# Kernel optimization log

Hardware: AMD Instinct MI355X
Metric: run time of the kernel (lower is better)

## Reference

```python
import jax, jax.numpy as jnp
import numpy as np

N = 50000   # nodes
E = 600000  # edges
D = 128     # in = hidden = out channels (must be equal per the cat/mean readout)
B = 4096    # number of lookup indices


def setup_inputs() -> dict:
    key = jax.random.key(0)
    ks = jax.random.split(key, 8)
    x = jax.random.normal(ks[0], (N, D), dtype=jnp.float32)
    edge_index = jax.random.randint(ks[1], (2, E), 0, N)
    edge_weight = jax.random.uniform(ks[2], (E,), dtype=jnp.float32)
    inputs_idx = jax.random.randint(ks[3], (B,), 0, N + 1)  # N is the appended zero row
    def lin_w(k, din, dout):
        return jax.random.normal(k, (din, dout), dtype=jnp.float32) / np.sqrt(din).astype(np.float32)
    W1 = lin_w(ks[4], D, D); b1 = jnp.zeros((D,), jnp.float32)
    W2 = lin_w(ks[5], D, D); b2 = jnp.zeros((D,), jnp.float32)
    W3 = lin_w(ks[6], D, D); b3 = jnp.zeros((D,), jnp.float32)
    return {"inputs_idx": inputs_idx, "x": x, "edge_index": edge_index,
            "edge_weight": edge_weight, "W1": W1, "b1": b1, "W2": W2,
            "b2": b2, "W3": W3, "b3": b3}


def gcn_conv(x, W, b, src, dst, w):
    # PyG GCNConv with add_self_loops=True (fill weight 1) and symmetric norm.
    deg = jnp.zeros((N,), x.dtype).at[dst].add(w) + 1.0  # self-loop contributes 1
    dinv = jax.lax.rsqrt(deg)
    norm = dinv[src] * w * dinv[dst]                      # [E]
    h = x @ W                                             # [N, D]
    agg = jax.ops.segment_sum(norm[:, None] * h[src], dst, num_segments=N)
    agg = agg + h * (dinv * dinv)[:, None]                # self-loop term: deg^-1 * h
    return agg + b


def lookup(x, inputs_idx):
    # append a zero row, then gather
    x_ = jnp.concatenate([x, jnp.zeros((1, x.shape[-1]), x.dtype)], axis=0)
    return x_[inputs_idx]  # [B, D]


def reference(inputs_idx, x, edge_index, edge_weight, W1, b1, W2, b2, W3, b3):
    src, dst = edge_index[0], edge_index[1]
    x1 = jax.nn.relu(gcn_conv(x, W1, b1, src, dst, edge_weight))
    x2 = jax.nn.relu(gcn_conv(x1, W2, b2, src, dst, edge_weight))
    x3 = jax.nn.relu(gcn_conv(x2, W3, b3, src, dst, edge_weight))
    e1 = lookup(x1, inputs_idx)
    e2 = lookup(x2, inputs_idx)
    e3 = lookup(x3, inputs_idx)
    # torch.cat([1,B,D]x3, dim=0).mean(0) == elementwise mean of the three
    return (e1 + e2 + e3) / 3.0
```

## Files before the change

### kernel.cpp

```cpp
#include <hip/hip_runtime.h>
#include <hip/hip_fp16.h>

#define D 128
#define STRIDE 48

typedef _Float16 f16x8 __attribute__((ext_vector_type(8)));
typedef float f32x4 __attribute__((ext_vector_type(4)));
struct h4 { __half2 a, b; };

__global__ __launch_bounds__(256) void zero_kernel(int* __restrict__ p, int n) {
  int i = blockIdx.x * 256 + threadIdx.x;
  if (i < n) p[i] = 0;
}

__global__ __launch_bounds__(256) void build_kernel(
    const int* __restrict__ ei, const float* __restrict__ ew,
    int* __restrict__ cnt, int2* __restrict__ pairs, int E) {
  int e = blockIdx.x * 256 + threadIdx.x;
  if (e >= E) return;
  int s = ei[e], d = ei[E + e];
  int rank = atomicAdd(&cnt[d], 1);
  if (rank < STRIDE) pairs[(size_t)d * STRIDE + rank] = make_int2(s, __float_as_int(ew[e]));
}

__global__ __launch_bounds__(256) void deg_dinv_kernel(
    int* __restrict__ cnt, const int2* __restrict__ pairs,
    float* __restrict__ dinv, int N) {
  int n = blockIdx.x * 4 + (threadIdx.x >> 6);
  int lane = threadIdx.x & 63;
  if (n >= N) return;
  int c = cnt[n];
  c = c < STRIDE ? c : STRIDE;
  float v = (lane < c) ? __int_as_float(pairs[(size_t)n * STRIDE + lane].y) : 0.f;
#pragma unroll
  for (int o = 32; o > 0; o >>= 1) v += __shfl_xor(v, o, 64);
  if (lane == 0) {
    dinv[n] = rsqrtf(v + 1.0f);
    cnt[n] = c;
  }
}

__global__ __launch_bounds__(256) void norm_kernel(
    const int* __restrict__ cnt, const float* __restrict__ dinv,
    int2* __restrict__ pairs, int N) {
  int n = blockIdx.x * 4 + (threadIdx.x >> 6);
  int lane = threadIdx.x & 63;
  if (n >= N) return;
  int c = cnt[n];
  float di = dinv[n];
  if (lane < c) {
    int2 p = pairs[(size_t)n * STRIDE + lane];
    p.y = __float_as_int(dinv[p.x] * __int_as_float(p.y) * di);
    pairs[(size_t)n * STRIDE + lane] = p;
  }
}

__global__ __launch_bounds__(256) void tohalf_kernel(
    const float* __restrict__ in, __half* __restrict__ out, int n4) {
  int t = blockIdx.x * 256 + threadIdx.x;
  if (t >= n4) return;
  float4 v = ((const float4*)in)[t];
  h4 o = {__floats2half2_rn(v.x, v.y), __floats2half2_rn(v.z, v.w)};
  ((h4*)out)[t] = o;
}

__global__ __launch_bounds__(256) void wtrans_kernel(
    const float* __restrict__ W1, const float* __restrict__ W2,
    const float* __restrict__ W3, __half* __restrict__ WT1,
    __half* __restrict__ WT2, __half* __restrict__ WT3) {
  int t = blockIdx.x * 256 + threadIdx.x;
  if (t >= 3 * D * D) return;
  int m = t >> 14;
  int i = t & (D * D - 1);
  int k = i >> 7, n = i & 127;
  const float* W = (m == 0) ? W1 : (m == 1) ? W2 : W3;
  __half* WT = (m == 0) ? WT1 : (m == 1) ? WT2 : WT3;
  WT[n * D + k] = __float2half(W[k * D + n]);
}

__global__ __launch_bounds__(256) void agg_kernel(
    const __half* __restrict__ x16, const float* __restrict__ dinv,
    const int* __restrict__ cnt, const int2* __restrict__ pairs,
    __half* __restrict__ agg16, int N) {
  int gw = (blockIdx.x * 256 + threadIdx.x) >> 6;
  int lane = threadIdx.x & 63;
  if (gw >= N) return;
  const __half2* xs = (const __half2*)x16;
  float di = dinv[gw];
  int c = cnt[gw];
  const int2* pr = pairs + (size_t)gw * STRIDE;
  float2 acc = __half22float2(xs[(size_t)gw * 64 + lane]);
  acc.x *= di * di;
  acc.y *= di * di;
  int e = 0;
  for (; e + 4 <= c; e += 4) {
    int2 p0 = pr[e], p1 = pr[e + 1], p2 = pr[e + 2], p3 = pr[e + 3];
    float n0 = __int_as_float(p0.y), n1 = __int_as_float(p1.y);
    float n2 = __int_as_float(p2.y), n3 = __int_as_float(p3.y);
    float2 v0 = __half22float2(xs[(size_t)p0.x * 64 + lane]);
    float2 v1 = __half22float2(xs[(size_t)p1.x * 64 + lane]);
    float2 v2 = __half22float2(xs[(size_t)p2.x * 64 + lane]);
    float2 v3 = __half22float2(xs[(size_t)p3.x * 64 + lane]);
    acc.x += n0 * v0.x + n1 * v1.x + n2 * v2.x + n3 * v3.x;
    acc.y += n0 * v0.y + n1 * v1.y + n2 * v2.y + n3 * v3.y;
  }
  for (; e < c; e++) {
    int2 p0 = pr[e];
    float n0 = __int_as_float(p0.y);
    float2 v0 = __half22float2(xs[(size_t)p0.x * 64 + lane]);
    acc.x += n0 * v0.x;
    acc.y += n0 * v0.y;
  }
  ((__half2*)agg16)[(size_t)gw * 64 + lane] = __floats2half2_rn(acc.x, acc.y);
}

__global__ __launch_bounds__(256) void gemm16(
    const __half* __restrict__ A16, const __half* __restrict__ WT,
    const float* __restrict__ bias, __half* __restrict__ out16, int n) {
  __shared__ __half Bs[D * D];
  const int tid = threadIdx.x;
  const int wid = tid >> 6;
  const int lane = tid & 63;
  const int l15 = lane & 15;
  const int lk = lane >> 4;
  const int rbase = blockIdx.x * 64 + wid * 16;

  f16x8 a[4];
  {
    int r = rbase + l15;
    bool ok = (r < n);
    const __half* arow = A16 + (size_t)r * D + lk * 8;
#pragma unroll
    for (int kk = 0; kk < 4; kk++) {
      f16x8 z = {0, 0, 0, 0, 0, 0, 0, 0};
      a[kk] = ok ? *(const f16x8*)(arow + kk * 32) : z;
    }
  }
  {
    const int4* src = (const int4*)WT;
#pragma unroll
    for (int i = 0; i < 8; i++) {
      int slot = tid + i * 256;
      int byte = slot << 4;
      int row = byte >> 8;
      int4 v = src[slot];
      *(int4*)((char*)Bs + (byte ^ ((row & 7) << 4))) = v;
    }
  }
  __syncthreads();

  f32x4 c[8];
#pragma unroll
  for (int nf = 0; nf < 8; nf++) c[nf] = (f32x4){0.f, 0.f, 0.f, 0.f};

#pragma unroll
  for (int kk = 0; kk < 4; kk++) {
#pragma unroll
    for (int nf = 0; nf < 8; nf++) {
      int byte = ((nf * 16 + l15) << 8) + (kk << 6) + (lk << 4);
      byte ^= (l15 & 7) << 4;
      f16x8 b = *(const f16x8*)((const char*)Bs + byte);
      c[nf] = __builtin_amdgcn_mfma_f32_16x16x32_f16(a[kk], b, c[nf], 0, 0, 0);
    }
  }

#pragma unroll
  for (int nf = 0; nf < 8; nf++) {
    float bv = bias[nf * 16 + l15];
    int r0 = rbase + lk * 4;
#pragma unroll
    for (int rg = 0; rg < 4; rg++) {
      int r = r0 + rg;
      if (r < n) {
        float v = fmaxf(c[nf][rg] + bv, 0.f);
        out16[(size_t)r * D + nf * 16 + l15] = __float2half(v);
      }
    }
  }
}

__global__ __launch_bounds__(256) void lookup_kernel(
    const __half* __restrict__ xl, const int* __restrict__ idx,
    float* __restrict__ out, int B, int N, int add) {
  int t = blockIdx.x * 256 + threadIdx.x;
  if (t >= B * 16) return;
  int b = t >> 4, c8 = t & 15;
  int id = idx[b];
  float4 o0 = make_float4(0.f, 0.f, 0.f, 0.f);
  float4 o1 = make_float4(0.f, 0.f, 0.f, 0.f);
  if ((unsigned)id < (unsigned)N) {
    int4 raw = *(const int4*)(xl + (size_t)id * D + c8 * 8);
    const __half2* h = (const __half2*)&raw;
    float2 f0 = __half22float2(h[0]);
    float2 f1 = __half22float2(h[1]);
    float2 f2 = __half22float2(h[2]);
    float2 f3 = __half22float2(h[3]);
    o0 = make_float4(f0.x, f0.y, f1.x, f1.y);
    o1 = make_float4(f2.x, f2.y, f3.x, f3.y);
  }
  const float s = 1.0f / 3.0f;
  float* op = out + (size_t)b * D + c8 * 8;
  if (add) {
    float4 p0 = *(float4*)op, p1 = *(float4*)(op + 4);
    p0.x += o0.x * s; p0.y += o0.y * s; p0.z += o0.z * s; p0.w += o0.w * s;
    p1.x += o1.x * s; p1.y += o1.y * s; p1.z += o1.z * s; p1.w += o1.w * s;
    *(float4*)op = p0; *(float4*)(op + 4) = p1;
  } else {
    float4 p0 = make_float4(o0.x * s, o0.y * s, o0.z * s, o0.w * s);
    float4 p1 = make_float4(o1.x * s, o1.y * s, o1.z * s, o1.w * s);
    *(float4*)op = p0; *(float4*)(op + 4) = p1;
  }
}


extern "C" void kernel_launch(void* const* d_in, const int* in_sizes, int n_in,
                              void* d_out, int out_size, void* d_ws, size_t ws_size,
                              hipStream_t stream) {
  const int*   inputs_idx  = (const int*)d_in[0];
  const float* x           = (const float*)d_in[1];
  const int*   edge_index  = (const int*)d_in[2];
  const float* edge_weight = (const float*)d_in[3];
  const float* W1 = (const float*)d_in[4];
  const float* b1 = (const float*)d_in[5];
  const float* W2 = (const float*)d_in[6];
  const float* b2 = (const float*)d_in[7];
  const float* W3 = (const float*)d_in[8];
  const float* b3 = (const float*)d_in[9];
  float* out = (float*)d_out;

  const int B = in_sizes[0];
  const int N = in_sizes[1] / D;
  const int E = in_sizes[3];
  (void)n_in; (void)out_size; (void)ws_size;

  char* p = (char*)d_ws;
  size_t off = 0;
  auto alloc = [&](size_t bytes) -> void* {
    void* r = p + off;
    off += (bytes + 255) & ~(size_t)255;
    return r;
  };
  int*    cnt   = (int*)alloc((size_t)N * 4);
  float*  dinv  = (float*)alloc((size_t)N * 4);
  int2*   pairs = (int2*)alloc((size_t)N * STRIDE * 8);
  __half* x16   = (__half*)alloc((size_t)N * D * 2);
  __half* aggT  = (__half*)alloc((size_t)N * D * 2);
  __half* oA    = (__half*)alloc((size_t)N * D * 2);
  __half* oB    = (__half*)alloc((size_t)N * D * 2);
  __half* WT1   = (__half*)alloc((size_t)D * D * 2);
  __half* WT2   = (__half*)alloc((size_t)D * D * 2);
  __half* WT3   = (__half*)alloc((size_t)D * D * 2);

  int eb = (E + 255) / 256;
  int wb = (N + 3) / 4;
  zero_kernel<<<(N + 255) / 256, 256, 0, stream>>>(cnt, N);
  build_kernel<<<eb, 256, 0, stream>>>(edge_index, edge_weight, cnt, pairs, E);
  deg_dinv_kernel<<<wb, 256, 0, stream>>>(cnt, pairs, dinv, N);
  norm_kernel<<<wb, 256, 0, stream>>>(cnt, dinv, pairs, N);
  int n4 = N * D / 4;
  tohalf_kernel<<<(n4 + 255) / 256, 256, 0, stream>>>(x, x16, n4);
  wtrans_kernel<<<(3 * D * D + 255) / 256, 256, 0, stream>>>(W1, W2, W3, WT1, WT2, WT3);

  int ab = (N + 3) / 4;
  int gb = (N + 63) / 64;
  int lb = (B * 16 + 255) / 256;

  agg_kernel<<<ab, 256, 0, stream>>>(x16, dinv, cnt, pairs, aggT, N);
  gemm16<<<gb, 256, 0, stream>>>(aggT, WT1, b1, oA, N);
  lookup_kernel<<<lb, 256, 0, stream>>>(oA, inputs_idx, out, B, N, 0);
  agg_kernel<<<ab, 256, 0, stream>>>(oA, dinv, cnt, pairs, aggT, N);
  gemm16<<<gb, 256, 0, stream>>>(aggT, WT2, b2, oB, N);
  lookup_kernel<<<lb, 256, 0, stream>>>(oB, inputs_idx, out, B, N, 1);
  agg_kernel<<<ab, 256, 0, stream>>>(oB, dinv, cnt, pairs, aggT, N);
  gemm16<<<gb, 256, 0, stream>>>(aggT, WT3, b3, oA, N);
  lookup_kernel<<<lb, 256, 0, stream>>>(oA, inputs_idx, out, B, N, 1);
}
```

Baseline: 205.8 us.

## Fuse neighbor aggregation and GEMM into one per-layer kernel via LDS

After: 387.4 us. 88.2% more time.

```diff
diff --git a/kernel.cpp b/kernel.cpp
--- a/kernel.cpp
+++ b/kernel.cpp
@@ -78,64 +78,18 @@
   WT[n * D + k] = __float2half(W[k * D + n]);
 }
 
-__global__ __launch_bounds__(256) void agg_kernel(
+__global__ __launch_bounds__(256) void layer_kernel(
     const __half* __restrict__ x16, const float* __restrict__ dinv,
     const int* __restrict__ cnt, const int2* __restrict__ pairs,
-    __half* __restrict__ agg16, int N) {
-  int gw = (blockIdx.x * 256 + threadIdx.x) >> 6;
-  int lane = threadIdx.x & 63;
-  if (gw >= N) return;
-  const __half2* xs = (const __half2*)x16;
-  float di = dinv[gw];
-  int c = cnt[gw];
-  const int2* pr = pairs + (size_t)gw * STRIDE;
-  float2 acc = __half22float2(xs[(size_t)gw * 64 + lane]);
-  acc.x *= di * di;
-  acc.y *= di * di;
-  int e = 0;
-  for (; e + 4 <= c; e += 4) {
-    int2 p0 = pr[e], p1 = pr[e + 1], p2 = pr[e + 2], p3 = pr[e + 3];
-    float n0 = __int_as_float(p0.y), n1 = __int_as_float(p1.y);
-    float n2 = __int_as_float(p2.y), n3 = __int_as_float(p3.y);
-    float2 v0 = __half22float2(xs[(size_t)p0.x * 64 + lane]);
-    float2 v1 = __half22float2(xs[(size_t)p1.x * 64 + lane]);
-    float2 v2 = __half22float2(xs[(size_t)p2.x * 64 + lane]);
-    float2 v3 = __half22float2(xs[(size_t)p3.x * 64 + lane]);
-    acc.x += n0 * v0.x + n1 * v1.x + n2 * v2.x + n3 * v3.x;
-    acc.y += n0 * v0.y + n1 * v1.y + n2 * v2.y + n3 * v3.y;
-  }
-  for (; e < c; e++) {
-    int2 p0 = pr[e];
-    float n0 = __int_as_float(p0.y);
-    float2 v0 = __half22float2(xs[(size_t)p0.x * 64 + lane]);
-    acc.x += n0 * v0.x;
-    acc.y += n0 * v0.y;
-  }
-  ((__half2*)agg16)[(size_t)gw * 64 + lane] = __floats2half2_rn(acc.x, acc.y);
-}
-
-__global__ __launch_bounds__(256) void gemm16(
-    const __half* __restrict__ A16, const __half* __restrict__ WT,
-    const float* __restrict__ bias, __half* __restrict__ out16, int n) {
+    const __half* __restrict__ WT, const float* __restrict__ bias,
+    __half* __restrict__ out16, int n) {
   __shared__ __half Bs[D * D];
+  __shared__ __half As[64 * D];
   const int tid = threadIdx.x;
   const int wid = tid >> 6;
   const int lane = tid & 63;
-  const int l15 = lane & 15;
-  const int lk = lane >> 4;
-  const int rbase = blockIdx.x * 64 + wid * 16;
-
-  f16x8 a[4];
-  {
-    int r = rbase + l15;
-    bool ok = (r < n);
-    const __half* arow = A16 + (size_t)r * D + lk * 8;
-#pragma unroll
-    for (int kk = 0; kk < 4; kk++) {
-      f16x8 z = {0, 0, 0, 0, 0, 0, 0, 0};
-      a[kk] = ok ? *(const f16x8*)(arow + kk * 32) : z;
-    }
-  }
+  const int rbase = blockIdx.x * 64;
+
   {
     const int4* src = (const int4*)WT;
 #pragma unroll
@@ -147,12 +101,59 @@
       *(int4*)((char*)Bs + (byte ^ ((row & 7) << 4))) = v;
     }
   }
+
+  const __half2* xs = (const __half2*)x16;
+#pragma unroll 1
+  for (int i = 0; i < 16; i++) {
+    int row = wid * 16 + i;
+    int node = rbase + row;
+    float2 acc = make_float2(0.f, 0.f);
+    if (node < n) {
+      float di = dinv[node];
+      int c = cnt[node];
+      const int2* pr = pairs + (size_t)node * STRIDE;
+      acc = __half22float2(xs[(size_t)node * 64 + lane]);
+      acc.x *= di * di;
+      acc.y *= di * di;
+      int e = 0;
+      for (; e + 4 <= c; e += 4) {
+        int2 p0 = pr[e], p1 = pr[e + 1], p2 = pr[e + 2], p3 = pr[e + 3];
+        float n0 = __int_as_float(p0.y), n1 = __int_as_float(p1.y);
+        float n2 = __int_as_float(p2.y), n3 = __int_as_float(p3.y);
+        float2 v0 = __half22float2(xs[(size_t)p0.x * 64 + lane]);
+        float2 v1 = __half22float2(xs[(size_t)p1.x * 64 + lane]);
+        float2 v2 = __half22float2(xs[(size_t)p2.x * 64 + lane]);
+        float2 v3 = __half22float2(xs[(size_t)p3.x * 64 + lane]);
+        acc.x += n0 * v0.x + n1 * v1.x + n2 * v2.x + n3 * v3.x;
+        acc.y += n0 * v0.y + n1 * v1.y + n2 * v2.y + n3 * v3.y;
+      }
+      for (; e < c; e++) {
+        int2 p0 = pr[e];
+        float n0 = __int_as_float(p0.y);
+        float2 v0 = __half22float2(xs[(size_t)p0.x * 64 + lane]);
+        acc.x += n0 * v0.x;
+        acc.y += n0 * v0.y;
+      }
+    }
+    int byte = (row << 8) + (lane << 2);
+    *(__half2*)((char*)As + (byte ^ ((row & 7) << 4))) = __floats2half2_rn(acc.x, acc.y);
+  }
   __syncthreads();
 
+  const int l15 = lane & 15;
+  const int lk = lane >> 4;
+  f16x8 a[4];
+  {
+    int row = wid * 16 + l15;
+#pragma unroll
+    for (int kk = 0; kk < 4; kk++) {
+      int byte = (row << 8) + (kk << 6) + (lk << 4);
+      a[kk] = *(const f16x8*)((const char*)As + (byte ^ ((row & 7) << 4)));
+    }
+  }
   f32x4 c[8];
 #pragma unroll
   for (int nf = 0; nf < 8; nf++) c[nf] = (f32x4){0.f, 0.f, 0.f, 0.f};
-
 #pragma unroll
   for (int kk = 0; kk < 4; kk++) {
 #pragma unroll
@@ -163,11 +164,10 @@
       c[nf] = __builtin_amdgcn_mfma_f32_16x16x32_f16(a[kk], b, c[nf], 0, 0, 0);
     }
   }
-
 #pragma unroll
   for (int nf = 0; nf < 8; nf++) {
     float bv = bias[nf * 16 + l15];
-    int r0 = rbase + lk * 4;
+    int r0 = rbase + wid * 16 + lk * 4;
 #pragma unroll
     for (int rg = 0; rg < 4; rg++) {
       int r = r0 + rg;
@@ -244,7 +244,6 @@
   float*  dinv  = (float*)alloc((size_t)N * 4);
   int2*   pairs = (int2*)alloc((size_t)N * STRIDE * 8);
   __half* x16   = (__half*)alloc((size_t)N * D * 2);
-  __half* aggT  = (__half*)alloc((size_t)N * D * 2);
   __half* oA    = (__half*)alloc((size_t)N * D * 2);
   __half* oB    = (__half*)alloc((size_t)N * D * 2);
   __half* WT1   = (__half*)alloc((size_t)D * D * 2);
@@ -257,21 +256,16 @@
   build_kernel<<<eb, 256, 0, stream>>>(edge_index, edge_weight, cnt, pairs, E);
   deg_dinv_kernel<<<wb, 256, 0, stream>>>(cnt, pairs, dinv, N);
   norm_kernel<<<wb, 256, 0, stream>>>(cnt, dinv, pairs, N);
-  int n4 = N * D / 4;
-  tohalf_kernel<<<(n4 + 255) / 256, 256, 0, stream>>>(x, x16, n4);
+  tohalf_kernel<<<(N * 32 + 255) / 256, 256, 0, stream>>>(x, x16, N * 32);
   wtrans_kernel<<<(3 * D * D + 255) / 256, 256, 0, stream>>>(W1, W2, W3, WT1, WT2, WT3);
 
-  int ab = (N + 3) / 4;
   int gb = (N + 63) / 64;
   int lb = (B * 16 + 255) / 256;
 
-  agg_kernel<<<ab, 256, 0, stream>>>(x16, dinv, cnt, pairs, aggT, N);
-  gemm16<<<gb, 256, 0, stream>>>(aggT, WT1, b1, oA, N);
+  layer_kernel<<<gb, 256, 0, stream>>>(x16, dinv, cnt, pairs, WT1, b1, oA, N);
   lookup_kernel<<<lb, 256, 0, stream>>>(oA, inputs_idx, out, B, N, 0);
-  agg_kernel<<<ab, 256, 0, stream>>>(oA, dinv, cnt, pairs, aggT, N);
-  gemm16<<<gb, 256, 0, stream>>>(aggT, WT2, b2, oB, N);
+  layer_kernel<<<gb, 256, 0, stream>>>(oA, dinv, cnt, pairs, WT2, b2, oB, N);
   lookup_kernel<<<lb, 256, 0, stream>>>(oB, inputs_idx, out, B, N, 1);
-  agg_kernel<<<ab, 256, 0, stream>>>(oB, dinv, cnt, pairs, aggT, N);
-  gemm16<<<gb, 256, 0, stream>>>(aggT, WT3, b3, oA, N);
+  layer_kernel<<<gb, 256, 0, stream>>>(oB, dinv, cnt, pairs, WT3, b3, oA, N);
   lookup_kernel<<<lb, 256, 0, stream>>>(oA, inputs_idx, out, B, N, 1);
 }
```

## Compute third GCN layer only for looked-up nodes

Applied to the files above, without the earlier changes.

After: 176.9 us. 14.1% less time.

```diff
diff --git a/kernel.cpp b/kernel.cpp
--- a/kernel.cpp
+++ b/kernel.cpp
@@ -114,6 +114,46 @@
   ((__half2*)agg16)[(size_t)gw * 64 + lane] = __floats2half2_rn(acc.x, acc.y);
 }
 
+__global__ __launch_bounds__(256) void agg_idx_kernel(
+    const __half* __restrict__ x16, const float* __restrict__ dinv,
+    const int* __restrict__ cnt, const int2* __restrict__ pairs,
+    const int* __restrict__ idx, __half* __restrict__ aggI, int B, int N) {
+  int gw = (blockIdx.x * 256 + threadIdx.x) >> 6;
+  int lane = threadIdx.x & 63;
+  if (gw >= B) return;
+  const __half2* xs = (const __half2*)x16;
+  float2 acc = make_float2(0.f, 0.f);
+  int node = idx[gw];
+  if ((unsigned)node < (unsigned)N) {
+    float di = dinv[node];
+    int c = cnt[node];
+    const int2* pr = pairs + (size_t)node * STRIDE;
+    acc = __half22float2(xs[(size_t)node * 64 + lane]);
+    acc.x *= di * di;
+    acc.y *= di * di;
+    int e = 0;
+    for (; e + 4 <= c; e += 4) {
+      int2 p0 = pr[e], p1 = pr[e + 1], p2 = pr[e + 2], p3 = pr[e + 3];
+      float n0 = __int_as_float(p0.y), n1 = __int_as_float(p1.y);
+      float n2 = __int_as_float(p2.y), n3 = __int_as_float(p3.y);
+      float2 v0 = __half22float2(xs[(size_t)p0.x * 64 + lane]);
+      float2 v1 = __half22float2(xs[(size_t)p1.x * 64 + lane]);
+      float2 v2 = __half22float2(xs[(size_t)p2.x * 64 + lane]);
+      float2 v3 = __half22float2(xs[(size_t)p3.x * 64 + lane]);
+      acc.x += n0 * v0.x + n1 * v1.x + n2 * v2.x + n3 * v3.x;
+      acc.y += n0 * v0.y + n1 * v1.y + n2 * v2.y + n3 * v3.y;
+    }
+    for (; e < c; e++) {
+      int2 p0 = pr[e];
+      float n0 = __int_as_float(p0.y);
+      float2 v0 = __half22float2(xs[(size_t)p0.x * 64 + lane]);
+      acc.x += n0 * v0.x;
+      acc.y += n0 * v0.y;
+    }
+  }
+  ((__half2*)aggI)[(size_t)gw * 64 + lane] = __floats2half2_rn(acc.x, acc.y);
+}
+
 __global__ __launch_bounds__(256) void gemm16(
     const __half* __restrict__ A16, const __half* __restrict__ WT,
     const float* __restrict__ bias, __half* __restrict__ out16, int n) {
@@ -212,6 +252,27 @@
   }
 }
 
+__global__ __launch_bounds__(256) void lookup_direct_kernel(
+    const __half* __restrict__ oC, const int* __restrict__ idx,
+    float* __restrict__ out, int B, int N) {
+  int t = blockIdx.x * 256 + threadIdx.x;
+  if (t >= B * 16) return;
+  int b = t >> 4, c8 = t & 15;
+  if ((unsigned)idx[b] >= (unsigned)N) return;
+  int4 raw = *(const int4*)(oC + (size_t)b * D + c8 * 8);
+  const __half2* h = (const __half2*)&raw;
+  float2 f0 = __half22float2(h[0]);
+  float2 f1 = __half22float2(h[1]);
+  float2 f2 = __half22float2(h[2]);
+  float2 f3 = __half22float2(h[3]);
+  const float s = 1.0f / 3.0f;
+  float* op = out + (size_t)b * D + c8 * 8;
+  float4 p0 = *(float4*)op, p1 = *(float4*)(op + 4);
+  p0.x += f0.x * s; p0.y += f0.y * s; p0.z += f1.x * s; p0.w += f1.y * s;
+  p1.x += f2.x * s; p1.y += f2.y * s; p1.z += f3.x * s; p1.w += f3.y * s;
+  *(float4*)op = p0; *(float4*)(op + 4) = p1;
+}
+
 
 extern "C" void kernel_launch(void* const* d_in, const int* in_sizes, int n_in,
                               void* d_out, int out_size, void* d_ws, size_t ws_size,
@@ -257,8 +318,7 @@
   build_kernel<<<eb, 256, 0, stream>>>(edge_index, edge_weight, cnt, pairs, E);
   deg_dinv_kernel<<<wb, 256, 0, stream>>>(cnt, pairs, dinv, N);
   norm_kernel<<<wb, 256, 0, stream>>>(cnt, dinv, pairs, N);
-  int n4 = N * D / 4;
-  tohalf_kernel<<<(n4 + 255) / 256, 256, 0, stream>>>(x, x16, n4);
+  tohalf_kernel<<<(N * 32 + 255) / 256, 256, 0, stream>>>(x, x16, N * 32);
   wtrans_kernel<<<(3 * D * D + 255) / 256, 256, 0, stream>>>(W1, W2, W3, WT1, WT2, WT3);
 
   int ab = (N + 3) / 4;
@@ -271,7 +331,9 @@
   agg_kernel<<<ab, 256, 0, stream>>>(oA, dinv, cnt, pairs, aggT, N);
   gemm16<<<gb, 256, 0, stream>>>(aggT, WT2, b2, oB, N);
   lookup_kernel<<<lb, 256, 0, stream>>>(oB, inputs_idx, out, B, N, 1);
-  agg_kernel<<<ab, 256, 0, stream>>>(oB, dinv, cnt, pairs, aggT, N);
-  gemm16<<<gb, 256, 0, stream>>>(aggT, WT3, b3, oA, N);
-  lookup_kernel<<<lb, 256, 0, stream>>>(oA, inputs_idx, out, B, N, 1);
-}
+  int ib = (B + 3) / 4;
+  int gb3 = (B + 63) / 64;
+  agg_idx_kernel<<<ib, 256, 0, stream>>>(oB, dinv, cnt, pairs, inputs_idx, aggT, B, N);
+  gemm16<<<gb3, 256, 0, stream>>>(aggT, WT3, b3, oA, B);
+  lookup_direct_kernel<<<lb, 256, 0, stream>>>(oA, inputs_idx, out, B, N);
+}
```
